# Performance work log

Measured on AMD Instinct MI355X. Metric: run time of the kernel, lower is better.

The kernel has to match this reference:

```python
import jax, jax.numpy as jnp
import numpy as np

B, D, K = 512, 128, 131072
TEMP = 0.07
PTR = 0  # queue_ptr starts at 0; B <= K so single contiguous write


def _normalize(x, axis):
    return x / jnp.linalg.norm(x, axis=axis, keepdims=True)


def setup_inputs() -> dict:
    key = jax.random.key(0)
    k = jax.random.split(key, 7)
    return {
        "predict0": jax.random.normal(k[0], (B, D), jnp.float32),
        "predict1": jax.random.normal(k[1], (B, D), jnp.float32),
        "project0": jax.random.normal(k[2], (B, D), jnp.float32),
        "project1": jax.random.normal(k[3], (B, D), jnp.float32),
        "queue": jax.random.normal(k[4], (D, K), jnp.float32),
        "queue_id": jax.random.randint(k[5], (K,), 0, 100000, jnp.int64) if jax.config.jax_enable_x64 else jax.random.randint(k[5], (K,), 0, 100000, jnp.int32),
        "ids": jax.random.randint(k[6], (B,), 0, 100000, jnp.int64) if jax.config.jax_enable_x64 else jax.random.randint(k[6], (B,), 0, 100000, jnp.int32),
    }


def _find_nn(proj, queue_n, queue_id, ids):
    # [B, K] similarity, mask out entries with same sample id, argmax, gather cols
    sim = proj @ queue_n                                   # [B, K]
    is_own = queue_id[None, :] == ids[:, None]             # [B, K]
    sim = jnp.where(is_own, jnp.float32(-1.0), sim)
    idx = jnp.argmax(sim, axis=1)                          # [B]
    return queue_n[:, idx]                                 # [D, B]


def _nnclr_loss(predicted, nn, temperature):
    # logits[i, j] = nn_i . predicted_j / T ; labels = arange(B)
    logits = (nn.T @ predicted.T) / temperature            # [B, B]
    logp = jax.nn.log_softmax(logits, axis=-1)
    return -jnp.mean(jnp.diagonal(logp))


def reference(predict0, predict1, project0, project1, queue, queue_id, ids):
    # forward_encoder's normalization (encoder itself is external and modeled out)
    p0 = _normalize(predict0, 1)
    p1 = _normalize(predict1, 1)
    z0 = _normalize(project0, 1)
    z1 = _normalize(project1, 1)
    queue_n = _normalize(queue, 0)  # queue stored normalized along dim 0

    # find_nn / queue are no_grad in the original
    nn0 = jax.lax.stop_gradient(_find_nn(jax.lax.stop_gradient(z0), queue_n, queue_id, ids))
    nn1 = jax.lax.stop_gradient(_find_nn(jax.lax.stop_gradient(z1), queue_n, queue_id, ids))

    loss0 = _nnclr_loss(p0, nn1, TEMP)
    loss1 = _nnclr_loss(p1, nn0, TEMP)
    loss = (loss0 + loss1) * 0.5

    # _dequeue_and_enqueue: ptr=0, B <= K -> contiguous slice write
    new_queue = jax.lax.dynamic_update_slice(queue_n, jax.lax.stop_gradient(z0.T), (0, PTR))
    new_queue_id = jax.lax.dynamic_update_slice(queue_id, ids, (PTR,))
    new_ptr = jnp.array((PTR + B) % K, dtype=queue_id.dtype)
    return loss, new_queue, new_queue_id, new_ptr
```

## Files before the change

### kernel.cpp

```cpp
#include <hip/hip_runtime.h>
#include <hip/hip_bf16.h>

typedef _Float16 half8 __attribute__((ext_vector_type(8)));
typedef _Float16 half4 __attribute__((ext_vector_type(4)));
typedef float f32x4 __attribute__((ext_vector_type(4)));

#define B 512
#define D 128
#define K 131072
#define TEMP 0.07f
#define NKB 256
#define KT_PER 32

#define INVN_OFF 0
#define Z0_OFF   131072
#define Z1_OFF   196608
#define P0_OFF   262144
#define P1_OFF   327680
#define ZF16_OFF 393216
#define QA_OFF   458752
#define PVAL_OFF 8847360
#define IDX_OFF  9373696
#define LP_OFF   9374720
#define IDM_OFF  9375744

__device__ __forceinline__ void gload_lds16(const _Float16* g, _Float16* l) {
  __builtin_amdgcn_global_load_lds(
      (const __attribute__((address_space(1))) unsigned int*)g,
      (__attribute__((address_space(3))) unsigned int*)l, 16, 0, 0);
}

__global__ __launch_bounds__(128) void rownorm_k(
    const float* __restrict__ p0, const float* __restrict__ p1,
    const float* __restrict__ z0, const float* __restrict__ z1,
    float* __restrict__ w, _Float16* __restrict__ zf16) {
  int row = blockIdx.x & (B - 1);
  int which = blockIdx.x >> 9;
  const float* src; float* dst;
  switch (which) {
    case 0: src = z0; dst = w + Z0_OFF; break;
    case 1: src = z1; dst = w + Z1_OFF; break;
    case 2: src = p0; dst = w + P0_OFF; break;
    default: src = p1; dst = w + P1_OFF; break;
  }
  int tid = threadIdx.x;
  float v = src[row * D + tid];
  float s = v * v;
  #pragma unroll
  for (int o = 32; o; o >>= 1) s += __shfl_xor(s, o);
  __shared__ float sm[2];
  if ((tid & 63) == 0) sm[tid >> 6] = s;
  __syncthreads();
  float inv = rsqrtf(sm[0] + sm[1]);
  float nv = v * inv;
  dst[row * D + tid] = nv;
  if (which < 2) zf16[(which * B + row) * D + tid] = (_Float16)nv;
}

__global__ __launch_bounds__(256) void idmask_k(
    const int* __restrict__ qid, const int* __restrict__ ids,
    unsigned short* __restrict__ idm) {
  __shared__ int sids[B];
  int tid = threadIdx.x;
  sids[tid] = ids[tid];
  sids[tid + 256] = ids[tid + 256];
  __syncthreads();
  int k = blockIdx.x * 256 + tid;
  int myq = qid[k];
  bool match = false;
  #pragma unroll 4
  for (int j = 0; j < B; j += 4) {
    int4 i4 = *(const int4*)&sids[j];
    match |= (myq == i4.x) | (myq == i4.y) | (myq == i4.z) | (myq == i4.w);
  }
  unsigned long long bal = __ballot(match);
  int lane = tid & 63;
  if ((lane & 15) == 0)
    idm[k >> 4] = (unsigned short)((bal >> lane) & 0xFFFFull);
}

__global__ __launch_bounds__(256) void colq_k(
    const float* __restrict__ q, const int* __restrict__ qid,
    const int* __restrict__ ids, const float* __restrict__ w_z0,
    float* __restrict__ invn, float* __restrict__ out,
    _Float16* __restrict__ qA) {
  __shared__ float psum[8][128];
  __shared__ float invs[128];
  __shared__ float sm2[2];
  __shared__ float fcol[128];
  __shared__ _Float16 tile[128][136];
  int tid = threadIdx.x;
  int kb = blockIdx.x;
  int k0 = kb * 128;
  int kc = tid & 31, dg = tid >> 5;

  float fqv = 0.f;
  if (kb > 4 && tid < 128) fqv = q[(size_t)tid * K + (k0 - 1)];

  float4 v[16];
  {
    float4 acc = {0.f, 0.f, 0.f, 0.f};
    #pragma unroll
    for (int i = 0; i < 16; i++) {
      int d = dg * 16 + i;
      v[i] = *(const float4*)(q + (size_t)d * K + k0 + kc * 4);
      acc.x = fmaf(v[i].x, v[i].x, acc.x); acc.y = fmaf(v[i].y, v[i].y, acc.y);
      acc.z = fmaf(v[i].z, v[i].z, acc.z); acc.w = fmaf(v[i].w, v[i].w, acc.w);
    }
    *(float4*)&psum[dg][kc * 4] = acc;
  }
  __syncthreads();
  if (tid < 128) {
    float s = 0.f;
    #pragma unroll
    for (int g2 = 0; g2 < 8; g2++) s += psum[g2][tid];
    float inv = rsqrtf(s);
    invs[tid] = inv;
    invn[k0 + tid] = inv;
    int kk = k0 + tid;
    out[1 + (size_t)D * K + kk] = (float)((kk < B) ? ids[kk] : qid[kk]);
  }
  if (kb > 4 && tid < 128) {
    float s2 = fqv * fqv;
    #pragma unroll
    for (int o = 32; o; o >>= 1) s2 += __shfl_xor(s2, o);
    if ((tid & 63) == 0) sm2[tid >> 6] = s2;
  }
  __syncthreads();
  if (kb > 4) {
    if (tid < 128) fcol[tid] = fqv * rsqrtf(sm2[0] + sm2[1]);
  } else if (kb == 4) {
    if (tid < 32)
      *(float4*)&fcol[tid * 4] = *(const float4*)(w_z0 + (size_t)511 * D + tid * 4);
  }
  __syncthreads();

  float4 iv = *(const float4*)&invs[kc * 4];
  if (kb >= 4) {
    #pragma unroll
    for (int i = 0; i < 16; i++) {
      int d = dg * 16 + i;
      float o0 = v[i].x * iv.x, o1 = v[i].y * iv.y;
      float o2 = v[i].z * iv.z, o3 = v[i].w * iv.w;
      half4 t = {(_Float16)o0, (_Float16)o1, (_Float16)o2, (_Float16)o3};
      *(half4*)&tile[d][kc * 4] = t;
      float p3 = __shfl_up(o3, 1);
      float x0 = (kc == 0) ? fcol[d] : p3;
      float4 st = {x0, o0, o1, o2};
      *(float4*)(out + (size_t)d * K + k0 + kc * 4) = st;
      if (kb == 1023 && kc == 31)
        out[1 + (size_t)d * K + (K - 1)] = o3;
    }
  } else {
    #pragma unroll
    for (int i = 0; i < 16; i++) {
      int d = dg * 16 + i;
      float o0 = v[i].x * iv.x, o1 = v[i].y * iv.y;
      float o2 = v[i].z * iv.z, o3 = v[i].w * iv.w;
      half4 t = {(_Float16)o0, (_Float16)o1, (_Float16)o2, (_Float16)o3};
      *(half4*)&tile[d][kc * 4] = t;
      float* oc = out + 1 + (size_t)d * K + k0 + kc * 4;
      int col = k0 + kc * 4;
      oc[0] = w_z0[(size_t)(col + 0) * D + d];
      oc[1] = w_z0[(size_t)(col + 1) * D + d];
      oc[2] = w_z0[(size_t)(col + 2) * D + d];
      oc[3] = w_z0[(size_t)(col + 3) * D + d];
    }
  }
  __syncthreads();
  {
    int dc = tid >> 6, l = tid & 63;
    int g = l >> 4, c = l & 15;
    #pragma unroll
    for (int kt = 0; kt < 8; kt++) {
      half8 f;
      #pragma unroll
      for (int i = 0; i < 8; i++) {
        int d = g * 4 + (i & 3) + ((i >> 2) << 4) + dc * 32;
        f[i] = tile[d][kt * 16 + c];
      }
      int ktg = kb * 8 + kt;
      *(half8*)(qA + (size_t)((ktg * 4 + dc) * 64 + l) * 8) = f;
    }
  }
}

#define PROCESS(AF, Q4) do { \
  _Pragma("unroll") \
  for (int nt = 0; nt < 4; nt++) { \
    f32x4 acc = {0.f, 0.f, 0.f, 0.f}; \
    _Pragma("unroll") \
    for (int dc = 0; dc < 4; dc++) \
      acc = __builtin_amdgcn_mfma_f32_16x16x32_f16(AF[dc], bf[nt][dc], acc, 0, 0, 0); \
    _Pragma("unroll") \
    for (int r = 0; r < 4; r++) { \
      int qv_ = (r == 0) ? Q4.x : (r == 1) ? Q4.y : (r == 2) ? Q4.z : Q4.w; \
      float sm_ = (qv_ == myid[nt]) ? -1.0f : acc[r]; \
      best[nt] = fmaxf(best[nt], sm_); \
    } \
  } \
} while (0)

#define PROCESS_CLEAN(AF) do { \
  _Pragma("unroll") \
  for (int nt = 0; nt < 4; nt++) { \
    f32x4 acc = {0.f, 0.f, 0.f, 0.f}; \
    _Pragma("unroll") \
    for (int dc = 0; dc < 4; dc++) \
      acc = __builtin_amdgcn_mfma_f32_16x16x32_f16(AF[dc], bf[nt][dc], acc, 0, 0, 0); \
    best[nt] = fmaxf(best[nt], \
        fmaxf(fmaxf(acc[0], acc[1]), fmaxf(acc[2], acc[3]))); \
  } \
} while (0)

__global__ __launch_bounds__(256) void nnsearch_k(
    const _Float16* __restrict__ qA, const _Float16* __restrict__ zf16,
    const int* __restrict__ qid, const int* __restrict__ ids,
    const unsigned short* __restrict__ idm, float* __restrict__ pval) {
  __shared__ __align__(16) _Float16 qtile[4][3][2048];
  __shared__ __align__(16) int qid_lds[512];
  __shared__ unsigned short qmask_lds[32];
  int tid = threadIdx.x;
  int flat = blockIdx.x;
  int cls = flat & 7;
  int kb = cls * 32 + (flat >> 5);
  int rg = (flat >> 3) & 3;
  int wave = tid >> 6, lane = tid & 63;
  int g = lane >> 4, c = lane & 15;
  int rowbase = rg * 256 + wave * 64;
  int kt0 = kb * KT_PER;

  #pragma unroll
  for (int j = 0; j < 2; j++)
    #pragma unroll
    for (int dc = 0; dc < 4; dc++)
      gload_lds16(qA + (size_t)(((kt0 + j) * 4 + dc) * 64 + lane) * 8,
                  &qtile[wave][j][dc * 512]);
  qid_lds[tid] = qid[kb * 512 + tid];
  qid_lds[tid + 256] = qid[kb * 512 + tid + 256];
  if (tid < 32) qmask_lds[tid] = idm[kt0 + tid];

  half8 bf[4][4];
  int myid[4];
  #pragma unroll
  for (int nt = 0; nt < 4; nt++) {
    int row = rowbase + nt * 16 + c;
    myid[nt] = ids[row & (B - 1)];
    #pragma unroll
    for (int dc = 0; dc < 4; dc++) {
      const _Float16* zr = zf16 + row * D + dc * 32 + g * 4;
      half4 lo = *(const half4*)zr;
      half4 hi = *(const half4*)(zr + 16);
      half8 f = {lo[0], lo[1], lo[2], lo[3], hi[0], hi[1], hi[2], hi[3]};
      bf[nt][dc] = f;
    }
  }
  __syncthreads();

  float best[4] = {-2.f, -2.f, -2.f, -2.f};
  for (int kt = 0; kt < KT_PER; kt++) {
    int cur = kt; if (cur >= 3) cur -= 3 * ((unsigned)(cur * 0x5556) >> 16);
    const _Float16* rb = &qtile[wave][cur][0];
    if (kt < KT_PER - 1) { asm volatile("s_waitcnt vmcnt(4)" ::: "memory"); }
    else                 { asm volatile("s_waitcnt vmcnt(0)" ::: "memory"); }
    __builtin_amdgcn_sched_barrier(0);
    half8 af[4];
    #pragma unroll
    for (int dc = 0; dc < 4; dc++)
      af[dc] = *(const half8*)(rb + dc * 512 + lane * 8);
    if (kt + 2 < KT_PER) {
      int nb = cur + 2; if (nb >= 3) nb -= 3;
      #pragma unroll
      for (int dc = 0; dc < 4; dc++)
        gload_lds16(qA + (size_t)(((kt0 + kt + 2) * 4 + dc) * 64 + lane) * 8,
                    &qtile[wave][nb][dc * 512]);
    }
    int ma = qmask_lds[kt];
    __builtin_amdgcn_s_setprio(1);
    if (ma) {
      int4 q4 = *(const int4*)&qid_lds[kt * 16 + g * 4];
      PROCESS(af, q4);
    } else {
      PROCESS_CLEAN(af);
    }
    __builtin_amdgcn_s_setprio(0);
  }

  #pragma unroll
  for (int nt = 0; nt < 4; nt++) {
    float v = best[nt];
    v = fmaxf(v, __shfl_xor(v, 16));
    v = fmaxf(v, __shfl_xor(v, 32));
    if (g == 0) {
      int row = rowbase + nt * 16 + c;
      pval[row * NKB + kb] = v;
    }
  }
}

__global__ __launch_bounds__(256) void nnpick_k(
    const float* __restrict__ pval, const _Float16* __restrict__ qA,
    const _Float16* __restrict__ zf16, const int* __restrict__ qid,
    const int* __restrict__ ids, int* __restrict__ idxout) {
  int row = blockIdx.x;
  int tid = threadIdx.x;
  int wave = tid >> 6, lane = tid & 63;
  int g = lane >> 4;
  __shared__ unsigned sv[4];
  __shared__ unsigned skb[4];
  __shared__ int s_kb;
  __shared__ float s_wv;
  {
    float a = pval[row * NKB + tid];
    unsigned v = (__float_as_uint(fmaf(a, 0.5f, 3.0f)) << 9) | (unsigned)(NKB - 1 - tid);
    #pragma unroll
    for (int o = 32; o; o >>= 1) {
      unsigned ov = __shfl_xor(v, o);
      v = v > ov ? v : ov;
    }
    if (lane == 0) sv[wave] = v;
  }
  __syncthreads();
  if (tid == 0) {
    unsigned v = sv[0];
    #pragma unroll
    for (int wv = 1; wv < 4; wv++) v = v > sv[wv] ? v : sv[wv];
    int kbw = (NKB - 1) - (int)(v & 0x1FFu);
    s_kb = kbw;
    s_wv = pval[row * NKB + kbw];
  }
  __syncthreads();
  int kb = s_kb;
  float wv = s_wv;
  int myid = ids[row & (B - 1)];

  half8 bf[4];
  #pragma unroll
  for (int dc = 0; dc < 4; dc++) {
    const _Float16* zr = zf16 + row * D + dc * 32 + g * 4;
    half4 lo = *(const half4*)zr;
    half4 hi = *(const half4*)(zr + 16);
    half8 f = {lo[0], lo[1], lo[2], lo[3], hi[0], hi[1], hi[2], hi[3]};
    bf[dc] = f;
  }

  unsigned kbest = 0x7FFFFFFFu;
  int ktbase = kb * KT_PER + wave * 8;
  for (int kt = 0; kt < 8; kt++) {
    int ktg = ktbase + kt;
    half8 af[4];
    #pragma unroll
    for (int dc = 0; dc < 4; dc++)
      af[dc] = *(const half8*)(qA + (size_t)((ktg * 4 + dc) * 64 + lane) * 8);
    int4 q4 = *(const int4*)(qid + ktg * 16 + g * 4);
    f32x4 acc = {0.f, 0.f, 0.f, 0.f};
    #pragma unroll
    for (int dc = 0; dc < 4; dc++)
      acc = __builtin_amdgcn_mfma_f32_16x16x32_f16(af[dc], bf[dc], acc, 0, 0, 0);
    #pragma unroll
    for (int r = 0; r < 4; r++) {
      int qv = (r == 0) ? q4.x : (r == 1) ? q4.y : (r == 2) ? q4.z : q4.w;
      float sm = (qv == myid) ? -1.0f : acc[r];
      if (sm == wv) {
        unsigned kk = (unsigned)(ktg * 16 + g * 4 + r);
        kbest = kbest < kk ? kbest : kk;
      }
    }
  }
  unsigned o1 = __shfl_xor(kbest, 16); kbest = kbest < o1 ? kbest : o1;
  unsigned o2 = __shfl_xor(kbest, 32); kbest = kbest < o2 ? kbest : o2;
  if (lane == 0) skb[wave] = kbest;
  __syncthreads();
  if (tid == 0) {
    unsigned v = skb[0];
    #pragma unroll
    for (int wv2 = 1; wv2 < 4; wv2++) v = v < skb[wv2] ? v : skb[wv2];
    idxout[row] = (int)(v < (K - 1) ? v : (K - 1));
  }
}

__global__ __launch_bounds__(256) void loss_k(
    const float* __restrict__ q, const float* __restrict__ invn,
    const int* __restrict__ idxout, const float* __restrict__ w,
    float* __restrict__ lpart) {
  int i0 = blockIdx.x * 8;
  int v = blockIdx.y;
  int tid = threadIdx.x;
  __shared__ float nns[8][D];
  __shared__ float rm[8][4], re[8][4], sdlds[8];
  #pragma unroll
  for (int ii = 0; ii < 4; ii++) {
    int i = ii * 2 + (tid >> 7);
    int d = tid & 127;
    int nnidx = idxout[(v ? 0 : B) + i0 + i];
    nns[i][d] = q[(size_t)d * K + nnidx] * invn[nnidx];
  }
  __syncthreads();
  const float* pr = w + (v ? P1_OFF : P0_OFF);
  const float* r0 = pr + tid * D;
  const float* r1 = pr + (tid + 256) * D;
  float a0[8] = {0, 0, 0, 0, 0, 0, 0, 0};
  float a1[8] = {0, 0, 0, 0, 0, 0, 0, 0};
  for (int d = 0; d < D; d += 4) {
    float4 x0 = *(const float4*)(r0 + d);
    float4 x1 = *(const float4*)(r1 + d);
    #pragma unroll
    for (int i = 0; i < 8; i++) {
      float4 n = *(const float4*)&nns[i][d];
      a0[i] = fmaf(x0.x, n.x, a0[i]); a0[i] = fmaf(x0.y, n.y, a0[i]);
      a0[i] = fmaf(x0.z, n.z, a0[i]); a0[i] = fmaf(x0.w, n.w, a0[i]);
      a1[i] = fmaf(x1.x, n.x, a1[i]); a1[i] = fmaf(x1.y, n.y, a1[i]);
      a1[i] = fmaf(x1.z, n.z, a1[i]); a1[i] = fmaf(x1.w, n.w, a1[i]);
    }
  }
  #pragma unroll
  for (int i = 0; i < 8; i++) {
    a0[i] *= (1.0f / TEMP);
    a1[i] *= (1.0f / TEMP);
  }
  #pragma unroll
  for (int i = 0; i < 8; i++) {
    int ig = i0 + i;
    if ((ig & 256) == 0) { if (tid == ig) sdlds[i] = a0[i]; }
    else { if (tid == (ig & 255)) sdlds[i] = a1[i]; }
  }
  int wv = tid >> 6;
  #pragma unroll
  for (int i = 0; i < 8; i++) {
    float m = fmaxf(a0[i], a1[i]);
    #pragma unroll
    for (int o = 32; o; o >>= 1) m = fmaxf(m, __shfl_xor(m, o));
    if ((tid & 63) == 0) rm[i][wv] = m;
  }
  __syncthreads();
  #pragma unroll
  for (int i = 0; i < 8; i++) {
    float m = fmaxf(fmaxf(rm[i][0], rm[i][1]), fmaxf(rm[i][2], rm[i][3]));
    float e = expf(a0[i] - m) + expf(a1[i] - m);
    #pragma unroll
    for (int o = 32; o; o >>= 1) e += __shfl_xor(e, o);
    if ((tid & 63) == 0) re[i][wv] = e;
  }
  __syncthreads();
  if (tid < 8) {
    int i = tid;
    float m = fmaxf(fmaxf(rm[i][0], rm[i][1]), fmaxf(rm[i][2], rm[i][3]));
    float s = re[i][0] + re[i][1] + re[i][2] + re[i][3];
    lpart[v * B + i0 + i] = sdlds[i] - m - logf(s);
  }
}

__global__ __launch_bounds__(256) void final_k(
    const float* __restrict__ lpart, float* __restrict__ out) {
  int tid = threadIdx.x;
  float s = lpart[tid] + lpart[tid + 256] + lpart[tid + 512] + lpart[tid + 768];
  #pragma unroll
  for (int o = 32; o; o >>= 1) s += __shfl_xor(s, o);
  __shared__ float sm[4];
  if ((tid & 63) == 0) sm[tid >> 6] = s;
  __syncthreads();
  if (tid == 0) {
    float total = sm[0] + sm[1] + sm[2] + sm[3];
    out[0] = -total * (1.0f / 1024.0f);
    out[1 + D * K + K] = 512.0f;
  }
}

extern "C" void kernel_launch(void* const* d_in, const int* in_sizes, int n_in,
                              void* d_out, int out_size, void* d_ws, size_t ws_size,
                              hipStream_t stream) {
  const float* p0 = (const float*)d_in[0];
  const float* p1 = (const float*)d_in[1];
  const float* z0 = (const float*)d_in[2];
  const float* z1 = (const float*)d_in[3];
  const float* q  = (const float*)d_in[4];
  const int* qid  = (const int*)d_in[5];
  const int* ids  = (const int*)d_in[6];
  float* out = (float*)d_out;
  float* w = (float*)d_ws;
  float* invn = w + INVN_OFF;
  _Float16* zf16 = (_Float16*)(w + ZF16_OFF);
  _Float16* qA   = (_Float16*)(w + QA_OFF);
  float* pval = w + PVAL_OFF;
  int* idxout = (int*)(w + IDX_OFF);
  float* lpart = w + LP_OFF;
  unsigned short* idm = (unsigned short*)(w + IDM_OFF);

  rownorm_k<<<2048, 128, 0, stream>>>(p0, p1, z0, z1, w, zf16);
  idmask_k<<<K / 256, 256, 0, stream>>>(qid, ids, idm);
  colq_k<<<K / 128, 256, 0, stream>>>(q, qid, ids, w + Z0_OFF, invn, out, qA);
  nnsearch_k<<<1024, 256, 0, stream>>>(qA, zf16, qid, ids, idm, pval);
  nnpick_k<<<1024, 256, 0, stream>>>(pval, qA, zf16, qid, ids, idxout);
  dim3 gl(B / 8, 2);
  loss_k<<<gl, 256, 0, stream>>>(q, invn, idxout, w, lpart);
  final_k<<<1, 256, 0, stream>>>(lpart, out);
}
```

Before: 130.4 us.

## Fuse queue normalization and NN search into one kernel, drop fp16 queue buffer

Merges the column-normalize/copy kernel with the nearest-neighbour search so each 1024-thread block normalizes a 128-column queue slice, builds MFMA fragments in LDS, and searches all 512 rows against it directly. This removes the global fp16 qA intermediate, which was a write followed by a re-read, and with it the LDS async prefetch pipeline. Partial maxima grow from 256 to 1024 per row, and nnpick now rescans the raw fp32 queue with strided loads to recompute the winning tile. The costs are lower occupancy with large blocks, a heavier per-block MFMA workload across 16 waves, and strided gathers in nnpick.

```diff
diff --git a/kernel.cpp b/kernel.cpp
--- a/kernel.cpp
+++ b/kernel.cpp
@@ -9,8 +9,7 @@
 #define D 128
 #define K 131072
 #define TEMP 0.07f
-#define NKB 256
-#define KT_PER 32
+#define NKB 1024
 
 #define INVN_OFF 0
 #define Z0_OFF   131072
@@ -18,17 +17,10 @@
 #define P0_OFF   262144
 #define P1_OFF   327680
 #define ZF16_OFF 393216
-#define QA_OFF   458752
-#define PVAL_OFF 8847360
-#define IDX_OFF  9373696
-#define LP_OFF   9374720
-#define IDM_OFF  9375744
-
-__device__ __forceinline__ void gload_lds16(const _Float16* g, _Float16* l) {
-  __builtin_amdgcn_global_load_lds(
-      (const __attribute__((address_space(1))) unsigned int*)g,
-      (__attribute__((address_space(3))) unsigned int*)l, 16, 0, 0);
-}
+#define PVAL_OFF 458752
+#define IDX_OFF  1507328
+#define LP_OFF   1508352
+#define IDM_OFF  1509376
 
 __global__ __launch_bounds__(128) void rownorm_k(
     const float* __restrict__ p0, const float* __restrict__ p1,
@@ -77,112 +69,6 @@
   int lane = tid & 63;
   if ((lane & 15) == 0)
     idm[k >> 4] = (unsigned short)((bal >> lane) & 0xFFFFull);
-}
-
-__global__ __launch_bounds__(256) void colq_k(
-    const float* __restrict__ q, const int* __restrict__ qid,
-    const int* __restrict__ ids, const float* __restrict__ w_z0,
-    float* __restrict__ invn, float* __restrict__ out,
-    _Float16* __restrict__ qA) {
-  __shared__ float psum[8][128];
-  __shared__ float invs[128];
-  __shared__ float sm2[2];
-  __shared__ float fcol[128];
-  __shared__ _Float16 tile[128][136];
-  int tid = threadIdx.x;
-  int kb = blockIdx.x;
-  int k0 = kb * 128;
-  int kc = tid & 31, dg = tid >> 5;
-
-  float fqv = 0.f;
-  if (kb > 4 && tid < 128) fqv = q[(size_t)tid * K + (k0 - 1)];
-
-  float4 v[16];
-  {
-    float4 acc = {0.f, 0.f, 0.f, 0.f};
-    #pragma unroll
-    for (int i = 0; i < 16; i++) {
-      int d = dg * 16 + i;
-      v[i] = *(const float4*)(q + (size_t)d * K + k0 + kc * 4);
-      acc.x = fmaf(v[i].x, v[i].x, acc.x); acc.y = fmaf(v[i].y, v[i].y, acc.y);
-      acc.z = fmaf(v[i].z, v[i].z, acc.z); acc.w = fmaf(v[i].w, v[i].w, acc.w);
-    }
-    *(float4*)&psum[dg][kc * 4] = acc;
-  }
-  __syncthreads();
-  if (tid < 128) {
-    float s = 0.f;
-    #pragma unroll
-    for (int g2 = 0; g2 < 8; g2++) s += psum[g2][tid];
-    float inv = rsqrtf(s);
-    invs[tid] = inv;
-    invn[k0 + tid] = inv;
-    int kk = k0 + tid;
-    out[1 + (size_t)D * K + kk] = (float)((kk < B) ? ids[kk] : qid[kk]);
-  }
-  if (kb > 4 && tid < 128) {
-    float s2 = fqv * fqv;
-    #pragma unroll
-    for (int o = 32; o; o >>= 1) s2 += __shfl_xor(s2, o);
-    if ((tid & 63) == 0) sm2[tid >> 6] = s2;
-  }
-  __syncthreads();
-  if (kb > 4) {
-    if (tid < 128) fcol[tid] = fqv * rsqrtf(sm2[0] + sm2[1]);
-  } else if (kb == 4) {
-    if (tid < 32)
-      *(float4*)&fcol[tid * 4] = *(const float4*)(w_z0 + (size_t)511 * D + tid * 4);
-  }
-  __syncthreads();
-
-  float4 iv = *(const float4*)&invs[kc * 4];
-  if (kb >= 4) {
-    #pragma unroll
-    for (int i = 0; i < 16; i++) {
-      int d = dg * 16 + i;
-      float o0 = v[i].x * iv.x, o1 = v[i].y * iv.y;
-      float o2 = v[i].z * iv.z, o3 = v[i].w * iv.w;
-      half4 t = {(_Float16)o0, (_Float16)o1, (_Float16)o2, (_Float16)o3};
-      *(half4*)&tile[d][kc * 4] = t;
-      float p3 = __shfl_up(o3, 1);
-      float x0 = (kc == 0) ? fcol[d] : p3;
-      float4 st = {x0, o0, o1, o2};
-      *(float4*)(out + (size_t)d * K + k0 + kc * 4) = st;
-      if (kb == 1023 && kc == 31)
-        out[1 + (size_t)d * K + (K - 1)] = o3;
-    }
-  } else {
-    #pragma unroll
-    for (int i = 0; i < 16; i++) {
-      int d = dg * 16 + i;
-      float o0 = v[i].x * iv.x, o1 = v[i].y * iv.y;
-      float o2 = v[i].z * iv.z, o3 = v[i].w * iv.w;
-      half4 t = {(_Float16)o0, (_Float16)o1, (_Float16)o2, (_Float16)o3};
-      *(half4*)&tile[d][kc * 4] = t;
-      float* oc = out + 1 + (size_t)d * K + k0 + kc * 4;
-      int col = k0 + kc * 4;
-      oc[0] = w_z0[(size_t)(col + 0) * D + d];
-      oc[1] = w_z0[(size_t)(col + 1) * D + d];
-      oc[2] = w_z0[(size_t)(col + 2) * D + d];
-      oc[3] = w_z0[(size_t)(col + 3) * D + d];
-    }
-  }
-  __syncthreads();
-  {
-    int dc = tid >> 6, l = tid & 63;
-    int g = l >> 4, c = l & 15;
-    #pragma unroll
-    for (int kt = 0; kt < 8; kt++) {
-      half8 f;
-      #pragma unroll
-      for (int i = 0; i < 8; i++) {
-        int d = g * 4 + (i & 3) + ((i >> 2) << 4) + dc * 32;
-        f[i] = tile[d][kt * 16 + c];
-      }
-      int ktg = kb * 8 + kt;
-      *(half8*)(qA + (size_t)((ktg * 4 + dc) * 64 + l) * 8) = f;
-    }
-  }
 }
 
 #define PROCESS(AF, Q4) do { \
@@ -213,33 +99,125 @@
   } \
 } while (0)
 
-__global__ __launch_bounds__(256) void nnsearch_k(
-    const _Float16* __restrict__ qA, const _Float16* __restrict__ zf16,
-    const int* __restrict__ qid, const int* __restrict__ ids,
-    const unsigned short* __restrict__ idm, float* __restrict__ pval) {
-  __shared__ __align__(16) _Float16 qtile[4][3][2048];
-  __shared__ __align__(16) int qid_lds[512];
-  __shared__ unsigned short qmask_lds[32];
-  int tid = threadIdx.x;
-  int flat = blockIdx.x;
-  int cls = flat & 7;
-  int kb = cls * 32 + (flat >> 5);
-  int rg = (flat >> 3) & 3;
+__global__ __launch_bounds__(1024) void fused_k(
+    const float* __restrict__ q, const int* __restrict__ qid,
+    const int* __restrict__ ids, const float* __restrict__ w_z0,
+    const _Float16* __restrict__ zf16, const unsigned short* __restrict__ idm,
+    float* __restrict__ invn, float* __restrict__ out,
+    float* __restrict__ pval) {
+  __shared__ __align__(16) char smem_raw[32768];
+  float (*psum)[128] = (float (*)[128])smem_raw;
+  _Float16* fragbuf = (_Float16*)smem_raw;
+  __shared__ _Float16 tile[128][136];
+  __shared__ float invs[128];
+  __shared__ float sm2[2];
+  __shared__ float fcol[128];
+  __shared__ __align__(16) int qid_lds[128];
+  __shared__ unsigned short qmask_lds[8];
+  int tid = threadIdx.x;
+  int kb = blockIdx.x;
+  int k0 = kb * 128;
+  int kc = tid & 31, dg = tid >> 5;
+
+  float fqv = 0.f;
+  if (kb > 4 && tid < 128) fqv = q[(size_t)tid * K + (k0 - 1)];
+  if (tid < 128) qid_lds[tid] = qid[k0 + tid];
+  if (tid < 8) qmask_lds[tid] = idm[kb * 8 + tid];
+
+  float4 v[4];
+  {
+    float4 acc = {0.f, 0.f, 0.f, 0.f};
+    #pragma unroll
+    for (int i = 0; i < 4; i++) {
+      int d = dg + i * 32;
+      v[i] = *(const float4*)(q + (size_t)d * K + k0 + kc * 4);
+      acc.x = fmaf(v[i].x, v[i].x, acc.x); acc.y = fmaf(v[i].y, v[i].y, acc.y);
+      acc.z = fmaf(v[i].z, v[i].z, acc.z); acc.w = fmaf(v[i].w, v[i].w, acc.w);
+    }
+    *(float4*)&psum[dg][kc * 4] = acc;
+  }
+  __syncthreads();
+  if (tid < 128) {
+    float s = 0.f;
+    #pragma unroll
+    for (int g2 = 0; g2 < 32; g2++) s += psum[g2][tid];
+    float inv = rsqrtf(s);
+    invs[tid] = inv;
+    invn[k0 + tid] = inv;
+    int kk = k0 + tid;
+    out[1 + (size_t)D * K + kk] = (float)((kk < B) ? ids[kk] : qid[kk]);
+  }
+  if (kb > 4 && tid < 128) {
+    float s2 = fqv * fqv;
+    #pragma unroll
+    for (int o = 32; o; o >>= 1) s2 += __shfl_xor(s2, o);
+    if ((tid & 63) == 0) sm2[tid >> 6] = s2;
+  }
+  __syncthreads();
+  if (kb > 4) {
+    if (tid < 128) fcol[tid] = fqv * rsqrtf(sm2[0] + sm2[1]);
+  } else if (kb == 4) {
+    if (tid < 32)
+      *(float4*)&fcol[tid * 4] = *(const float4*)(w_z0 + (size_t)511 * D + tid * 4);
+  }
+  __syncthreads();
+
+  {
+    float4 iv = *(const float4*)&invs[kc * 4];
+    if (kb >= 4) {
+      #pragma unroll
+      for (int i = 0; i < 4; i++) {
+        int d = dg + i * 32;
+        float o0 = v[i].x * iv.x, o1 = v[i].y * iv.y;
+        float o2 = v[i].z * iv.z, o3 = v[i].w * iv.w;
+        half4 t = {(_Float16)o0, (_Float16)o1, (_Float16)o2, (_Float16)o3};
+        *(half4*)&tile[d][kc * 4] = t;
+        float p3 = __shfl_up(o3, 1);
+        float x0 = (kc == 0) ? fcol[d] : p3;
+        float4 st = {x0, o0, o1, o2};
+        *(float4*)(out + (size_t)d * K + k0 + kc * 4) = st;
+        if (kb == 1023 && kc == 31)
+          out[1 + (size_t)d * K + (K - 1)] = o3;
+      }
+    } else {
+      #pragma unroll
+      for (int i = 0; i < 4; i++) {
+        int d = dg + i * 32;
+        float o0 = v[i].x * iv.x, o1 = v[i].y * iv.y;
+        float o2 = v[i].z * iv.z, o3 = v[i].w * iv.w;
+        half4 t = {(_Float16)o0, (_Float16)o1, (_Float16)o2, (_Float16)o3};
+        *(half4*)&tile[d][kc * 4] = t;
+        float* oc = out + 1 + (size_t)d * K + k0 + kc * 4;
+        int col = k0 + kc * 4;
+        oc[0] = w_z0[(size_t)(col + 0) * D + d];
+        oc[1] = w_z0[(size_t)(col + 1) * D + d];
+        oc[2] = w_z0[(size_t)(col + 2) * D + d];
+        oc[3] = w_z0[(size_t)(col + 3) * D + d];
+      }
+    }
+  }
+  __syncthreads();
+
+  #pragma unroll
+  for (int u0 = 0; u0 < 2; u0++) {
+    int u = tid + u0 * 1024;
+    int kt = u >> 8;
+    int r2 = u & 255;
+    int dc = r2 >> 6, l = r2 & 63;
+    int g2 = l >> 4, c2 = l & 15;
+    half8 f;
+    #pragma unroll
+    for (int i = 0; i < 8; i++) {
+      int d = g2 * 4 + (i & 3) + ((i >> 2) << 4) + dc * 32;
+      f[i] = tile[d][kt * 16 + c2];
+    }
+    *(half8*)(fragbuf + (size_t)((kt * 4 + dc) * 64 + l) * 8) = f;
+  }
+  __syncthreads();
+
   int wave = tid >> 6, lane = tid & 63;
   int g = lane >> 4, c = lane & 15;
-  int rowbase = rg * 256 + wave * 64;
-  int kt0 = kb * KT_PER;
-
-  #pragma unroll
-  for (int j = 0; j < 2; j++)
-    #pragma unroll
-    for (int dc = 0; dc < 4; dc++)
-      gload_lds16(qA + (size_t)(((kt0 + j) * 4 + dc) * 64 + lane) * 8,
-                  &qtile[wave][j][dc * 512]);
-  qid_lds[tid] = qid[kb * 512 + tid];
-  qid_lds[tid + 256] = qid[kb * 512 + tid + 256];
-  if (tid < 32) qmask_lds[tid] = idm[kt0 + tid];
-
+  int rowbase = wave * 64;
   half8 bf[4][4];
   int myid[4];
   #pragma unroll
@@ -255,26 +233,12 @@
       bf[nt][dc] = f;
     }
   }
-  __syncthreads();
-
   float best[4] = {-2.f, -2.f, -2.f, -2.f};
-  for (int kt = 0; kt < KT_PER; kt++) {
-    int cur = kt; if (cur >= 3) cur -= 3 * ((unsigned)(cur * 0x5556) >> 16);
-    const _Float16* rb = &qtile[wave][cur][0];
-    if (kt < KT_PER - 1) { asm volatile("s_waitcnt vmcnt(4)" ::: "memory"); }
-    else                 { asm volatile("s_waitcnt vmcnt(0)" ::: "memory"); }
-    __builtin_amdgcn_sched_barrier(0);
+  for (int kt = 0; kt < 8; kt++) {
     half8 af[4];
     #pragma unroll
     for (int dc = 0; dc < 4; dc++)
-      af[dc] = *(const half8*)(rb + dc * 512 + lane * 8);
-    if (kt + 2 < KT_PER) {
-      int nb = cur + 2; if (nb >= 3) nb -= 3;
-      #pragma unroll
-      for (int dc = 0; dc < 4; dc++)
-        gload_lds16(qA + (size_t)(((kt0 + kt + 2) * 4 + dc) * 64 + lane) * 8,
-                    &qtile[wave][nb][dc * 512]);
-    }
+      af[dc] = *(const half8*)(fragbuf + (size_t)((kt * 4 + dc) * 64 + lane) * 8);
     int ma = qmask_lds[kt];
     __builtin_amdgcn_s_setprio(1);
     if (ma) {
@@ -285,53 +249,66 @@
     }
     __builtin_amdgcn_s_setprio(0);
   }
-
   #pragma unroll
   for (int nt = 0; nt < 4; nt++) {
-    float v = best[nt];
-    v = fmaxf(v, __shfl_xor(v, 16));
-    v = fmaxf(v, __shfl_xor(v, 32));
+    float vv = best[nt];
+    vv = fmaxf(vv, __shfl_xor(vv, 16));
+    vv = fmaxf(vv, __shfl_xor(vv, 32));
     if (g == 0) {
       int row = rowbase + nt * 16 + c;
-      pval[row * NKB + kb] = v;
+      pval[(size_t)row * NKB + kb] = vv;
     }
   }
 }
 
 __global__ __launch_bounds__(256) void nnpick_k(
-    const float* __restrict__ pval, const _Float16* __restrict__ qA,
-    const _Float16* __restrict__ zf16, const int* __restrict__ qid,
-    const int* __restrict__ ids, int* __restrict__ idxout) {
+    const float* __restrict__ pval, const float* __restrict__ q,
+    const float* __restrict__ invn, const _Float16* __restrict__ zf16,
+    const int* __restrict__ qid, const int* __restrict__ ids,
+    int* __restrict__ idxout) {
   int row = blockIdx.x;
   int tid = threadIdx.x;
   int wave = tid >> 6, lane = tid & 63;
-  int g = lane >> 4;
-  __shared__ unsigned sv[4];
+  int g = lane >> 4, c = lane & 15;
+  __shared__ float svf[4];
   __shared__ unsigned skb[4];
+  __shared__ float s_wv;
   __shared__ int s_kb;
-  __shared__ float s_wv;
+  const float* p = pval + (size_t)row * NKB;
+  float v0 = p[tid], v1 = p[tid + 256], v2 = p[tid + 512], v3 = p[tid + 768];
   {
-    float a = pval[row * NKB + tid];
-    unsigned v = (__float_as_uint(fmaf(a, 0.5f, 3.0f)) << 9) | (unsigned)(NKB - 1 - tid);
+    float m = fmaxf(fmaxf(v0, v1), fmaxf(v2, v3));
+    #pragma unroll
+    for (int o = 32; o; o >>= 1) m = fmaxf(m, __shfl_xor(m, o));
+    if (lane == 0) svf[wave] = m;
+  }
+  __syncthreads();
+  float wv = fmaxf(fmaxf(svf[0], svf[1]), fmaxf(svf[2], svf[3]));
+  if (tid == 0) s_wv = wv;
+  {
+    unsigned kbest = 0xFFFFFFFFu;
+    if (v0 == wv) kbest = (unsigned)tid;
+    if (v1 == wv) kbest = kbest < (unsigned)(tid + 256) ? kbest : (unsigned)(tid + 256);
+    if (v2 == wv) kbest = kbest < (unsigned)(tid + 512) ? kbest : (unsigned)(tid + 512);
+    if (v3 == wv) kbest = kbest < (unsigned)(tid + 768) ? kbest : (unsigned)(tid + 768);
     #pragma unroll
     for (int o = 32; o; o >>= 1) {
-      unsigned ov = __shfl_xor(v, o);
-      v = v > ov ? v : ov;
-    }
-    if (lane == 0) sv[wave] = v;
+      unsigned ov = __shfl_xor(kbest, o);
+      kbest = kbest < ov ? kbest : ov;
+    }
+    if (lane == 0) skb[wave] = kbest;
   }
   __syncthreads();
   if (tid == 0) {
-    unsigned v = sv[0];
-    #pragma unroll
-    for (int wv = 1; wv < 4; wv++) v = v > sv[wv] ? v : sv[wv];
-    int kbw = (NKB - 1) - (int)(v & 0x1FFu);
-    s_kb = kbw;
-    s_wv = pval[row * NKB + kbw];
+    unsigned kbw = skb[0];
+    #pragma unroll
+    for (int wv2 = 1; wv2 < 4; wv2++) kbw = kbw < skb[wv2] ? kbw : skb[wv2];
+    s_kb = (int)kbw;
   }
   __syncthreads();
   int kb = s_kb;
-  float wv = s_wv;
+  float wval = s_wv;
+  int k0 = kb * 128;
   int myid = ids[row & (B - 1)];
 
   half8 bf[4];
@@ -345,14 +322,23 @@
   }
 
   unsigned kbest = 0x7FFFFFFFu;
-  int ktbase = kb * KT_PER + wave * 8;
-  for (int kt = 0; kt < 8; kt++) {
-    int ktg = ktbase + kt;
+  #pragma unroll
+  for (int kt2 = 0; kt2 < 2; kt2++) {
+    int ktl = wave * 2 + kt2;
+    int kk = k0 + ktl * 16 + c;
+    float invk = invn[kk];
     half8 af[4];
     #pragma unroll
-    for (int dc = 0; dc < 4; dc++)
-      af[dc] = *(const half8*)(qA + (size_t)((ktg * 4 + dc) * 64 + lane) * 8);
-    int4 q4 = *(const int4*)(qid + ktg * 16 + g * 4);
+    for (int dc = 0; dc < 4; dc++) {
+      half8 f;
+      #pragma unroll
+      for (int i = 0; i < 8; i++) {
+        int d = g * 4 + (i & 3) + ((i >> 2) << 4) + dc * 32;
+        f[i] = (_Float16)(q[(size_t)d * K + kk] * invk);
+      }
+      af[dc] = f;
+    }
+    int4 q4 = *(const int4*)(qid + k0 + ktl * 16 + g * 4);
     f32x4 acc = {0.f, 0.f, 0.f, 0.f};
     #pragma unroll
     for (int dc = 0; dc < 4; dc++)
@@ -361,9 +347,9 @@
     for (int r = 0; r < 4; r++) {
       int qv = (r == 0) ? q4.x : (r == 1) ? q4.y : (r == 2) ? q4.z : q4.w;
       float sm = (qv == myid) ? -1.0f : acc[r];
-      if (sm == wv) {
-        unsigned kk = (unsigned)(ktg * 16 + g * 4 + r);
-        kbest = kbest < kk ? kbest : kk;
+      if (sm == wval) {
+        unsigned kg = (unsigned)(k0 + ktl * 16 + g * 4 + r);
+        kbest = kbest < kg ? kbest : kg;
       }
     }
   }
@@ -372,10 +358,10 @@
   if (lane == 0) skb[wave] = kbest;
   __syncthreads();
   if (tid == 0) {
-    unsigned v = skb[0];
-    #pragma unroll
-    for (int wv2 = 1; wv2 < 4; wv2++) v = v < skb[wv2] ? v : skb[wv2];
-    idxout[row] = (int)(v < (K - 1) ? v : (K - 1));
+    unsigned vv = skb[0];
+    #pragma unroll
+    for (int wv2 = 1; wv2 < 4; wv2++) vv = vv < skb[wv2] ? vv : skb[wv2];
+    idxout[row] = (int)(vv < (K - 1) ? vv : (K - 1));
   }
 }
 
@@ -480,7 +466,6 @@
   float* w = (float*)d_ws;
   float* invn = w + INVN_OFF;
   _Float16* zf16 = (_Float16*)(w + ZF16_OFF);
-  _Float16* qA   = (_Float16*)(w + QA_OFF);
   float* pval = w + PVAL_OFF;
   int* idxout = (int*)(w + IDX_OFF);
   float* lpart = w + LP_OFF;
@@ -488,9 +473,9 @@
 
   rownorm_k<<<2048, 128, 0, stream>>>(p0, p1, z0, z1, w, zf16);
   idmask_k<<<K / 256, 256, 0, stream>>>(qid, ids, idm);
-  colq_k<<<K / 128, 256, 0, stream>>>(q, qid, ids, w + Z0_OFF, invn, out, qA);
-  nnsearch_k<<<1024, 256, 0, stream>>>(qA, zf16, qid, ids, idm, pval);
-  nnpick_k<<<1024, 256, 0, stream>>>(pval, qA, zf16, qid, ids, idxout);
+  fused_k<<<1024, 1024, 0, stream>>>(q, qid, ids, w + Z0_OFF, zf16, idm,
+                                     invn, out, pval);
+  nnpick_k<<<1024, 256, 0, stream>>>(pval, q, invn, zf16, qid, ids, idxout);
   dim3 gl(B / 8, 2);
   loss_k<<<gl, 256, 0, stream>>>(q, invn, idxout, w, lpart);
   final_k<<<1, 256, 0, stream>>>(lpart, out);
```

After: 146.4 us. +12.2%, slower.
